# Optimization experiments

Hardware: AMD Instinct MI355X
Metric: run time of the kernel (lower is better)

Reference implementation:

```python
import jax, jax.numpy as jnp
import numpy as np

NUM_USER = 20000
NUM_ITEM = 40000
N_NODES = NUM_USER + NUM_ITEM
DIM = 64
V_DIM = 2048
T_DIM = 768
N_EDGES = 1_000_000
K_USER = 40
K_ITEM = 10
N_LAYERS = 2


def setup_inputs() -> dict:
    key = jax.random.key(0)
    ks = iter(jax.random.split(key, 32))

    def xavier(shape):
        s = (2.0 / (shape[0] + shape[-1])) ** 0.5
        return jax.random.normal(next(ks), shape, jnp.float32) * s

    # bipartite user-item interactions, doubled (undirected), as in DRAGON.__init__
    u = jax.random.randint(next(ks), (N_EDGES,), 0, NUM_USER)
    it = jax.random.randint(next(ks), (N_EDGES,), NUM_USER, N_NODES)
    edge_index = jnp.stack([jnp.concatenate([u, it]), jnp.concatenate([it, u])])

    v_feat = jax.random.normal(next(ks), (NUM_ITEM, V_DIM), jnp.float32)
    t_feat = jax.random.normal(next(ks), (NUM_ITEM, T_DIM), jnp.float32)

    # KNN item-item adjacency (top-10 per row) with symmetric-normalized values,
    # mirroring get_knn_adj_mat/compute_normalized_laplacian
    rows = jnp.repeat(jnp.arange(NUM_ITEM), K_ITEM)
    cols = jax.random.randint(next(ks), (NUM_ITEM * K_ITEM,), 0, NUM_ITEM)
    mm_indices = jnp.stack([rows, cols])
    row_sum = jax.ops.segment_sum(jnp.ones(NUM_ITEM * K_ITEM, jnp.float32), rows,
                                  num_segments=NUM_ITEM) + 1e-7
    rinv = row_sum ** -0.5
    mm_values = rinv[rows] * rinv[cols]

    user_graph = jax.random.randint(next(ks), (NUM_USER, K_USER), 0, NUM_USER)
    user_weight_matrix = jax.nn.softmax(
        jax.random.normal(next(ks), (NUM_USER, K_USER), jnp.float32), axis=1)
    weight_u = jax.nn.softmax(
        jax.random.normal(next(ks), (NUM_USER, 2, 1), jnp.float32), axis=1)

    return {
        'edge_index': edge_index,
        'v_feat': v_feat, 't_feat': t_feat,
        'v_pref': xavier((NUM_USER, DIM)), 't_pref': xavier((NUM_USER, DIM)),
        'v_mlp1_w': xavier((V_DIM, 4 * DIM)), 'v_mlp1_b': jnp.zeros(4 * DIM, jnp.float32),
        'v_mlp2_w': xavier((4 * DIM, DIM)), 'v_mlp2_b': jnp.zeros(DIM, jnp.float32),
        't_mlp1_w': xavier((T_DIM, 4 * DIM)), 't_mlp1_b': jnp.zeros(4 * DIM, jnp.float32),
        't_mlp2_w': xavier((4 * DIM, DIM)), 't_mlp2_b': jnp.zeros(DIM, jnp.float32),
        'v_conv_w': xavier((DIM, DIM)), 'v_conv_b': jnp.zeros(DIM, jnp.float32),
        't_conv_w': xavier((DIM, DIM)), 't_conv_b': jnp.zeros(DIM, jnp.float32),
        'weight_u': weight_u,
        'user_graph': user_graph,
        'user_weight_matrix': user_weight_matrix,
        'mm_indices': mm_indices,
        'mm_values': mm_values,
    }


def _l2n(x):
    n = jnp.linalg.norm(x, axis=-1, keepdims=True)
    return x / jnp.maximum(n, 1e-12)


def reference(edge_index, v_feat, t_feat, v_pref, t_pref,
              v_mlp1_w, v_mlp1_b, v_mlp2_w, v_mlp2_b,
              t_mlp1_w, t_mlp1_b, t_mlp2_w, t_mlp2_b,
              v_conv_w, v_conv_b, t_conv_w, t_conv_b,
              weight_u, user_graph, user_weight_matrix,
              mm_indices, mm_values):
    seg = jax.ops.segment_sum
    # GCNConv normalization with self-loops (shared by both branches)
    sl = jnp.arange(N_NODES)
    src = jnp.concatenate([edge_index[0], sl])
    dst = jnp.concatenate([edge_index[1], sl])
    deg = seg(jnp.ones_like(dst, dtype=jnp.float32), dst, num_segments=N_NODES)
    dinv = deg ** -0.5
    norm = (dinv[src] * dinv[dst])[:, None]

    def conv(x, w, b):  # out[dst] += norm * (x @ w)[src], then bias
        return seg(norm * (x @ w)[src], dst, num_segments=N_NODES) + b

    def branch(feat, pref, w1, b1, w2, b2, cw, cb):
        temp = jax.nn.leaky_relu(feat @ w1 + b1) @ w2 + b2  # [I, D]
        x = _l2n(jnp.concatenate([pref, temp], axis=0))      # [N, D]
        h = conv(x, cw, cb)
        h1 = conv(h, cw, cb)
        return x + h + h1

    v_rep = branch(v_feat, v_pref, v_mlp1_w, v_mlp1_b, v_mlp2_w, v_mlp2_b, v_conv_w, v_conv_b)
    t_rep = branch(t_feat, t_pref, t_mlp1_w, t_mlp1_b, t_mlp2_w, t_mlp2_b, t_conv_w, t_conv_b)

    representation = jnp.concatenate([v_rep, t_rep], axis=1)  # [N, 2D]
    wu = weight_u[:, :, 0]  # [U, 2]
    user_rep = jnp.concatenate([wu[:, 0:1] * v_rep[:NUM_USER],
                                wu[:, 1:2] * t_rep[:NUM_USER]], axis=1)  # [U, 2D]
    item_rep = representation[NUM_USER:]  # [I, 2D]

    # User_Graph_sample: weighted sum over sampled user neighborhoods
    h_u = jnp.einsum('uk,ukd->ud', user_weight_matrix, user_rep[user_graph])
    user_rep = user_rep + h_u

    # n_layers of sparse Laplacian propagation over KNN item-item graph
    row, col = mm_indices[0], mm_indices[1]
    h_i = item_rep
    for _ in range(N_LAYERS):
        h_i = seg(mm_values[:, None] * h_i[col], row, num_segments=NUM_ITEM)
    item_rep = item_rep + h_i

    return jnp.concatenate([user_rep, item_rep], axis=0)  # [N, 2D]
```

## Files before the change

kernel.cpp:

```cpp
#include <hip/hip_runtime.h>

#define NUSER 20000
#define NITEM 40000
#define NNODE 60000
#define DIM   64
#define NE    1000000
#define KUSER 40
#define KITEM 10

typedef __attribute__((ext_vector_type(8))) short short8v;
typedef __attribute__((ext_vector_type(4))) float floatx4;

__device__ inline short bf16rne(float f) {
    unsigned u = __builtin_bit_cast(unsigned, f);
    unsigned r = (u + 0x7fffu + ((u >> 16) & 1u)) >> 16;
    return (short)r;
}
__device__ inline unsigned cvt_pk_bf16(float lo, float hi) {
    unsigned r;
    asm("v_cvt_pk_bf16_f32 %0, %1, %2" : "=v"(r) : "v"(lo), "v"(hi));
    return r;
}
__device__ inline float bflo(unsigned v) { return __builtin_bit_cast(float, v << 16); }
__device__ inline float bfhi(unsigned v) { return __builtin_bit_cast(float, v & 0xffff0000u); }

__global__ __launch_bounds__(256) void k_count(const int* __restrict__ dst, int* __restrict__ cnt, int n) {
    int i = blockIdx.x * 256 + threadIdx.x;
    if (i < n) atomicAdd(&cnt[dst[i]], 1);
}

__global__ __launch_bounds__(256) void k_dinv(const int* __restrict__ cnt, float* __restrict__ dinv) {
    int i = blockIdx.x * 256 + threadIdx.x;
    if (i < NNODE) dinv[i] = 1.0f / sqrtf((float)(cnt[i] + 1));
}

__global__ __launch_bounds__(256) void k_scanA(const int* __restrict__ v, int* __restrict__ excl,
                                               int* __restrict__ bsum, int n) {
    __shared__ int s[256];
    int t = threadIdx.x, i = blockIdx.x * 256 + t;
    int orig = (i < n) ? v[i] : 0;
    s[t] = orig; __syncthreads();
    #pragma unroll
    for (int off = 1; off < 256; off <<= 1) {
        int u = (t >= off) ? s[t - off] : 0;
        __syncthreads();
        s[t] += u;
        __syncthreads();
    }
    if (i < n) excl[i] = s[t] - orig;
    if (t == 255) bsum[blockIdx.x] = s[255];
}

__global__ __launch_bounds__(256) void k_scanB(int* __restrict__ bsum, int nb) {
    __shared__ int s[256];
    int t = threadIdx.x;
    int orig = (t < nb) ? bsum[t] : 0;
    s[t] = orig; __syncthreads();
    #pragma unroll
    for (int off = 1; off < 256; off <<= 1) {
        int u = (t >= off) ? s[t - off] : 0;
        __syncthreads();
        s[t] += u;
        __syncthreads();
    }
    if (t < nb) bsum[t] = s[t] - orig;
}

__global__ __launch_bounds__(256) void k_scanC(int* __restrict__ excl, const int* __restrict__ bsum,
                                               int* __restrict__ cursor, int n) {
    int i = blockIdx.x * 256 + threadIdx.x;
    if (i < n) {
        int v = excl[i] + bsum[blockIdx.x];
        excl[i] = v;
        cursor[i] = v;
    }
    if (i == 0) excl[n] = 2 * NE;
}

__global__ __launch_bounds__(256) void k_fill(const int* __restrict__ src, const int* __restrict__ dst,
                                              const float* __restrict__ dinv, int* __restrict__ cursor,
                                              unsigned* __restrict__ csr_pkd, int n) {
    int i = blockIdx.x * 256 + threadIdx.x;
    if (i >= n) return;
    int s = src[i], d = dst[i];
    unsigned pk = ((unsigned)(unsigned short)bf16rne(dinv[s]) << 16) | (unsigned)s;
    int pos = atomicAdd(&cursor[d], 1);
    csr_pkd[pos] = pk;
}

__global__ __launch_bounds__(256) void k_transpose_bf16(const float* __restrict__ B, short* __restrict__ Btb,
                                                        int K, int N) {
    __shared__ float s[16][17];
    int t = threadIdx.x, tx = t & 15, ty = t >> 4;
    int k0 = blockIdx.x * 16, n0 = blockIdx.y * 16;
    s[ty][tx] = B[(size_t)(k0 + ty) * N + n0 + tx];
    __syncthreads();
    int k = k0 + tx, n = n0 + ty;
    Btb[(size_t)(k >> 5) * (N * 32) + n * 32 + (k & 31)] = bf16rne(s[tx][ty]);
}

#define AP   40
#define MIDP 264
__global__ __launch_bounds__(256) void mlp_fused(const float* __restrict__ A, const short* __restrict__ B1t,
                                                 const float* __restrict__ b1, const short* __restrict__ B2t,
                                                 const float* __restrict__ b2, float* __restrict__ X, int K) {
    __shared__ short smem[2 * 64 * AP + 2 * 256 * AP];
    short* As = smem;
    short* Bs = smem + 2 * 64 * AP;
    const int tid = threadIdx.x;
    const int lane = tid & 63, wid = tid >> 6;
    const int rowBase = blockIdx.x * 64;

    const int sar = tid >> 2, sac = (tid & 3) * 8;
    const float* aptr = A + (size_t)(rowBase + sar) * K + sac;

    const int fk = (lane >> 4) * 8;
    const int faoff = (lane & 15) * AP + fk;
    const int fboff = (wid * 64 + (lane & 15)) * AP + fk;

    floatx4 acc[4][4];
    #pragma unroll
    for (int m = 0; m < 4; m++)
        #pragma unroll
        for (int n = 0; n < 4; n++) acc[m][n] = (floatx4)0.f;

    float4 ra0, ra1;
    short8v rb[4];
    const int nk = K >> 5;

    auto ldg = [&](int ks) {
        const float* ap = aptr + ks * 32;
        ra0 = *(const float4*)(ap);
        ra1 = *(const float4*)(ap + 4);
        const short* bsrc = B1t + (size_t)ks * 8192 + tid * 8;
        #pragma unroll
        for (int it = 0; it < 4; it++) rb[it] = *(const short8v*)(bsrc + it * 2048);
    };
    auto stv = [&](int buf) {
        uint4 av;
        av.x = cvt_pk_bf16(ra0.x, ra0.y); av.y = cvt_pk_bf16(ra0.z, ra0.w);
        av.z = cvt_pk_bf16(ra1.x, ra1.y); av.w = cvt_pk_bf16(ra1.z, ra1.w);
        *(uint4*)&As[buf * (64 * AP) + sar * AP + sac] = av;
        #pragma unroll
        for (int it = 0; it < 4; it++)
            *(short8v*)&Bs[buf * (256 * AP) + (sar + it * 64) * AP + sac] = rb[it];
    };

    ldg(0); stv(0);
    __syncthreads();
    int cur = 0;
    for (int ks = 0; ks < nk; ++ks) {
        if (ks + 1 < nk) ldg(ks + 1);
        short8v a[4], b[4];
        #pragma unroll
        for (int m = 0; m < 4; m++) a[m] = *(const short8v*)&As[cur * (64 * AP) + faoff + m * 16 * AP];
        #pragma unroll
        for (int n = 0; n < 4; n++) b[n] = *(const short8v*)&Bs[cur * (256 * AP) + fboff + n * 16 * AP];
        #pragma unroll
        for (int m = 0; m < 4; m++)
            #pragma unroll
            for (int n = 0; n < 4; n++)
                acc[m][n] = __builtin_amdgcn_mfma_f32_16x16x32_bf16(a[m], b[n], acc[m][n], 0, 0, 0);
        if (ks + 1 < nk) stv(cur ^ 1);
        __syncthreads();
        cur ^= 1;
    }

    short* mid = Bs;
    float bcol[4];
    #pragma unroll
    for (int n = 0; n < 4; n++) bcol[n] = b1[wid * 64 + n * 16 + (lane & 15)];
    #pragma unroll
    for (int m = 0; m < 4; m++)
        #pragma unroll
        for (int n = 0; n < 4; n++)
            #pragma unroll
            for (int q = 0; q < 4; q++) {
                int row = m * 16 + (lane >> 4) * 4 + q;
                int col = wid * 64 + n * 16 + (lane & 15);
                float v = acc[m][n][q] + bcol[n];
                v = v > 0.f ? v : 0.01f * v;
                mid[row * MIDP + col] = bf16rne(v);
            }
    __syncthreads();

    floatx4 acc2[4];
    #pragma unroll
    for (int n2 = 0; n2 < 4; n2++) acc2[n2] = (floatx4)0.f;
    const int arow = wid * 16 + (lane & 15);
    #pragma unroll
    for (int ks2 = 0; ks2 < 8; ++ks2) {
        short8v af = *(const short8v*)&mid[arow * MIDP + ks2 * 32 + fk];
        const short* bp = B2t + ks2 * 2048 + fk;
        short8v bf4[4];
        #pragma unroll
        for (int n2 = 0; n2 < 4; n2++) bf4[n2] = *(const short8v*)(bp + (n2 * 16 + (lane & 15)) * 32);
        #pragma unroll
        for (int n2 = 0; n2 < 4; n2++)
            acc2[n2] = __builtin_amdgcn_mfma_f32_16x16x32_bf16(af, bf4[n2], acc2[n2], 0, 0, 0);
    }

    float b2c[4];
    #pragma unroll
    for (int n2 = 0; n2 < 4; n2++) b2c[n2] = b2[n2 * 16 + (lane & 15)];
    #pragma unroll
    for (int q = 0; q < 4; ++q) {
        float v[4]; float ss = 0.f;
        #pragma unroll
        for (int n2 = 0; n2 < 4; n2++) { v[n2] = acc2[n2][q] + b2c[n2]; ss += v[n2] * v[n2]; }
        ss += __shfl_xor(ss, 1, 64);
        ss += __shfl_xor(ss, 2, 64);
        ss += __shfl_xor(ss, 4, 64);
        ss += __shfl_xor(ss, 8, 64);
        float sc = 1.f / fmaxf(sqrtf(ss), 1e-12f);
        int grow = rowBase + wid * 16 + (lane >> 4) * 4 + q;
        #pragma unroll
        for (int n2 = 0; n2 < 4; n2++)
            X[(size_t)grow * 64 + n2 * 16 + (lane & 15)] = v[n2] * sc;
    }
}

__global__ __launch_bounds__(256) void k_l2n_pref(const float* __restrict__ prefv, const float* __restrict__ preft,
                                                  float* __restrict__ xv, float* __restrict__ xt) {
    int row = blockIdx.x * 4 + (threadIdx.x >> 6);
    int lane = threadIdx.x & 63;
    if (row >= NUSER) return;
    const float* p = blockIdx.y ? preft : prefv;
    float* x = blockIdx.y ? xt : xv;
    float v = p[(size_t)row * 64 + lane];
    float ss = v * v;
    #pragma unroll
    for (int off = 32; off >= 1; off >>= 1) ss += __shfl_xor(ss, off, 64);
    x[(size_t)row * 64 + lane] = v / fmaxf(sqrtf(ss), 1e-12f);
}

__global__ __launch_bounds__(256) void conv_dual(const float* __restrict__ A0, const float* __restrict__ A1,
                                                 int lda, const float* __restrict__ Bv, const float* __restrict__ Bt2,
                                                 unsigned short* __restrict__ Ch) {
    __shared__ float As2[16][65];
    __shared__ float Bs2[16][65];
    const float* A = blockIdx.y ? A1 : A0;
    const float* B = blockIdx.y ? Bt2 : Bv;
    const int colOff = (int)blockIdx.y * 64;
    const int tid = threadIdx.x;
    const int tx = tid & 15, ty = tid >> 4;
    const int rowBase = blockIdx.x * 64;
    float acc[4][4] = {};
    for (int k0 = 0; k0 < 64; k0 += 16) {
        {
            int r = tid >> 2, c = (tid & 3) * 4;
            int gr = rowBase + r;
            float4 v = make_float4(0.f, 0.f, 0.f, 0.f);
            if (gr < NNODE) v = *(const float4*)(A + (size_t)gr * lda + k0 + c);
            As2[c + 0][r] = v.x; As2[c + 1][r] = v.y; As2[c + 2][r] = v.z; As2[c + 3][r] = v.w;
        }
        {
            int r = tid >> 4, c = (tid & 15) * 4;
            float4 v = *(const float4*)(B + (size_t)(k0 + r) * 64 + c);
            Bs2[r][c + 0] = v.x; Bs2[r][c + 1] = v.y; Bs2[r][c + 2] = v.z; Bs2[r][c + 3] = v.w;
        }
        __syncthreads();
        #pragma unroll
        for (int k = 0; k < 16; k++) {
            float a[4], b[4];
            #pragma unroll
            for (int i = 0; i < 4; i++) a[i] = As2[k][ty * 4 + i];
            #pragma unroll
            for (int j = 0; j < 4; j++) b[j] = Bs2[k][tx * 4 + j];
            #pragma unroll
            for (int i = 0; i < 4; i++)
                #pragma unroll
                for (int j = 0; j < 4; j++) acc[i][j] += a[i] * b[j];
        }
        __syncthreads();
    }
    const int gr0 = rowBase + ty * 4, gc = tx * 4;
    #pragma unroll
    for (int i = 0; i < 4; i++) {
        if (gr0 + i >= NNODE) break;
        uint2 hh;
        hh.x = cvt_pk_bf16(acc[i][0], acc[i][1]);
        hh.y = cvt_pk_bf16(acc[i][2], acc[i][3]);
        *(uint2*)(Ch + (size_t)(gr0 + i) * 128 + colOff + gc) = hh;
    }
}

__device__ inline float2 gather_row(const int* rowptr, const unsigned* csr_pkd, const unsigned* gw2,
                                    int row, int lane, float dr) {
    int p0 = rowptr[row], p1 = rowptr[row + 1];
    unsigned sv = gw2[(size_t)row * 64 + lane];
    float ax0 = dr * bflo(sv), ay0 = dr * bfhi(sv);
    float ax1 = 0.f, ay1 = 0.f;
    for (int p = p0; p < p1; p += 64) {
        int c = p1 - p; if (c > 64) c = 64;
        unsigned pk = (lane < c) ? csr_pkd[p + lane] : 0u;
        int j = 0;
        for (; j + 4 <= c; j += 4) {
            unsigned e0 = __shfl(pk, j, 64),     e1 = __shfl(pk, j + 1, 64);
            unsigned e2 = __shfl(pk, j + 2, 64), e3 = __shfl(pk, j + 3, 64);
            unsigned v0 = gw2[(size_t)(e0 & 0xffffu) * 64 + lane];
            unsigned v1 = gw2[(size_t)(e1 & 0xffffu) * 64 + lane];
            unsigned v2 = gw2[(size_t)(e2 & 0xffffu) * 64 + lane];
            unsigned v3 = gw2[(size_t)(e3 & 0xffffu) * 64 + lane];
            float w0 = bfhi(e0), w1 = bfhi(e1), w2 = bfhi(e2), w3 = bfhi(e3);
            ax0 += w0 * bflo(v0); ay0 += w0 * bfhi(v0);
            ax1 += w1 * bflo(v1); ay1 += w1 * bfhi(v1);
            ax0 += w2 * bflo(v2); ay0 += w2 * bfhi(v2);
            ax1 += w3 * bflo(v3); ay1 += w3 * bfhi(v3);
        }
        for (; j < c; ++j) {
            unsigned e = __shfl(pk, j, 64);
            unsigned v = gw2[(size_t)(e & 0xffffu) * 64 + lane];
            float w = bfhi(e);
            ax0 += w * bflo(v); ay0 += w * bfhi(v);
        }
    }
    float2 r; r.x = ax0 + ax1; r.y = ay0 + ay1;
    return r;
}

__global__ __launch_bounds__(256) void k_gather2(const int* __restrict__ rowptr, const unsigned* __restrict__ csr_pkd,
                                                 const float* __restrict__ dinv, const unsigned* __restrict__ gw2,
                                                 const float* __restrict__ cbv, const float* __restrict__ cbt,
                                                 float* __restrict__ h2) {
    int row = blockIdx.x * 4 + (threadIdx.x >> 6);
    int lane = threadIdx.x & 63;
    if (row >= NNODE) return;
    float dr = dinv[row];
    float2 g = gather_row(rowptr, csr_pkd, gw2, row, lane, dr);
    int c0 = 2 * lane;
    float b0 = (c0 < 64) ? cbv[c0] : cbt[c0 - 64];
    float b1 = (c0 + 1 < 64) ? cbv[c0 + 1] : cbt[c0 + 1 - 64];
    float2 r;
    r.x = b0 + dr * g.x;
    r.y = b1 + dr * g.y;
    *(float2*)(h2 + (size_t)row * 128 + c0) = r;
}

__global__ __launch_bounds__(256) void k_gather2_rep(const int* __restrict__ rowptr, const unsigned* __restrict__ csr_pkd,
                                                     const float* __restrict__ dinv, const unsigned* __restrict__ gw2,
                                                     const float* __restrict__ cbv, const float* __restrict__ cbt,
                                                     const float* __restrict__ xv, const float* __restrict__ xt,
                                                     const float* __restrict__ h2, const float* __restrict__ weight_u,
                                                     float* __restrict__ rep0, unsigned* __restrict__ rep_bf) {
    int row = blockIdx.x * 4 + (threadIdx.x >> 6);
    int lane = threadIdx.x & 63;
    if (row >= NNODE) return;
    float dr = dinv[row];
    float2 g = gather_row(rowptr, csr_pkd, gw2, row, lane, dr);
    int c0 = 2 * lane;
    float b0 = (c0 < 64) ? cbv[c0] : cbt[c0 - 64];
    float b1 = (c0 + 1 < 64) ? cbv[c0 + 1] : cbt[c0 + 1 - 64];
    float h12x = b0 + dr * g.x;
    float h12y = b1 + dr * g.y;
    const float* x = (lane < 32) ? xv : xt;
    float2 xp = *(const float2*)(x + (size_t)row * 64 + (c0 & 63));
    float2 hp = *(const float2*)(h2 + (size_t)row * 128 + c0);
    float w = (row < NUSER) ? weight_u[row * 2 + (lane >> 5)] : 1.0f;
    float2 rp;
    rp.x = w * (xp.x + hp.x + h12x);
    rp.y = w * (xp.y + hp.y + h12y);
    *(float2*)(rep0 + (size_t)row * 128 + c0) = rp;
    rep_bf[(size_t)row * 64 + lane] = cvt_pk_bf16(rp.x, rp.y);
}

#define UBLK (NUSER * 64 / 256)
__global__ __launch_bounds__(256) void k_user_item1(const float* __restrict__ rep0, const unsigned* __restrict__ rep_bf,
                                                    const int* __restrict__ ug, const float* __restrict__ uwm,
                                                    const int* __restrict__ mm_col, const float* __restrict__ mm_values,
                                                    float* __restrict__ out, unsigned* __restrict__ tmp_bf) {
    int bid = blockIdx.x;
    if (bid < UBLK) {
        int id = bid * 256 + threadIdx.x;
        int u = id >> 6, lane = id & 63;
        float2 acc = *(const float2*)(rep0 + (size_t)u * 128 + 2 * lane);
        #pragma unroll 4
        for (int k = 0; k < KUSER; k++) {
            int nb = ug[u * KUSER + k];
            float w = uwm[u * KUSER + k];
            unsigned v = rep_bf[(size_t)nb * 64 + lane];
            acc.x += w * bflo(v);
            acc.y += w * bfhi(v);
        }
        *(float2*)(out + (size_t)u * 128 + 2 * lane) = acc;
    } else {
        int id = (bid - UBLK) * 256 + threadIdx.x;
        int r = id >> 6, lane = id & 63;
        float ax = 0.f, ay = 0.f;
        #pragma unroll
        for (int j = 0; j < KITEM; j++) {
            int c = mm_col[r * KITEM + j];
            float w = mm_values[r * KITEM + j];
            unsigned v = rep_bf[(size_t)(NUSER + c) * 64 + lane];
            ax += w * bflo(v);
            ay += w * bfhi(v);
        }
        tmp_bf[(size_t)r * 64 + lane] = cvt_pk_bf16(ax, ay);
    }
}

__global__ __launch_bounds__(256) void k_item2(const float* __restrict__ rep0, const unsigned* __restrict__ tmp_bf,
                                               const int* __restrict__ mm_col, const float* __restrict__ mm_values,
                                               float* __restrict__ out) {
    int id = blockIdx.x * 256 + threadIdx.x;
    int r = id >> 6, lane = id & 63;
    if (r >= NITEM) return;
    float ax = 0.f, ay = 0.f;
    #pragma unroll
    for (int j = 0; j < KITEM; j++) {
        int c = mm_col[r * KITEM + j];
        float w = mm_values[r * KITEM + j];
        unsigned v = tmp_bf[(size_t)c * 64 + lane];
        ax += w * bflo(v);
        ay += w * bfhi(v);
    }
    float2 base = *(const float2*)(rep0 + (size_t)(NUSER + r) * 128 + 2 * lane);
    float2 o;
    o.x = base.x + ax;
    o.y = base.y + ay;
    *(float2*)(out + (size_t)(NUSER + r) * 128 + 2 * lane) = o;
}

extern "C" void kernel_launch(void* const* d_in, const int* in_sizes, int n_in,
                              void* d_out, int out_size, void* d_ws, size_t ws_size,
                              hipStream_t stream) {
    const int*   edge_index = (const int*)d_in[0];
    const float* v_feat   = (const float*)d_in[1];
    const float* t_feat   = (const float*)d_in[2];
    const float* v_pref   = (const float*)d_in[3];
    const float* t_pref   = (const float*)d_in[4];
    const float* v_mlp1_w = (const float*)d_in[5];
    const float* v_mlp1_b = (const float*)d_in[6];
    const float* v_mlp2_w = (const float*)d_in[7];
    const float* v_mlp2_b = (const float*)d_in[8];
    const float* t_mlp1_w = (const float*)d_in[9];
    const float* t_mlp1_b = (const float*)d_in[10];
    const float* t_mlp2_w = (const float*)d_in[11];
    const float* t_mlp2_b = (const float*)d_in[12];
    const float* v_conv_w = (const float*)d_in[13];
    const float* v_conv_b = (const float*)d_in[14];
    const float* t_conv_w = (const float*)d_in[15];
    const float* t_conv_b = (const float*)d_in[16];
    const float* weight_u = (const float*)d_in[17];
    const int*   user_graph = (const int*)d_in[18];
    const float* uwm      = (const float*)d_in[19];
    const int*   mm_indices = (const int*)d_in[20];
    const float* mm_values  = (const float*)d_in[21];
    float* out = (float*)d_out;

    char* wsb = (char*)d_ws;
    size_t off = 0;
    auto alloc = [&](size_t bytes) -> void* {
        void* p = wsb + off;
        off = (off + bytes + 255) & ~(size_t)255;
        return p;
    };
    int*      cnt     = (int*)     alloc(NNODE * 4);
    float*    dinv    = (float*)   alloc(NNODE * 4);
    int*      rowptr  = (int*)     alloc((NNODE + 1) * 4);
    int*      bsum    = (int*)     alloc(256 * 4);
    int*      cursor  = (int*)     alloc(NNODE * 4);
    unsigned* csr_pkd = (unsigned*)alloc((size_t)2 * NE * 4);
    short*    Btw     = (short*)   alloc((size_t)2048 * 256 * 2);
    short*    W2b     = (short*)   alloc((size_t)256 * 64 * 2);
    float*    xv      = (float*)   alloc((size_t)NNODE * DIM * 4);
    float*    xt      = (float*)   alloc((size_t)NNODE * DIM * 4);
    unsigned short* gw2 = (unsigned short*)alloc((size_t)NNODE * 128 * 2);
    float*    h2      = (float*)   alloc((size_t)NNODE * 128 * 4);
    float*    rep0    = (float*)   alloc((size_t)NNODE * 128 * 4);
    unsigned* rep_bf  = (unsigned*)alloc((size_t)NNODE * 64 * 4);
    unsigned* tmp_bf  = (unsigned*)alloc((size_t)NITEM * 64 * 4);
    (void)ws_size; (void)n_in; (void)in_sizes; (void)out_size;

    const int* e_src = edge_index;
    const int* e_dst = edge_index + 2 * NE;
    const int* mm_col = mm_indices + NITEM * KITEM;

    const int NB = (NNODE + 255) / 256;

    hipMemsetAsync(cnt, 0, NNODE * 4, stream);
    k_count<<<(2 * NE + 255) / 256, 256, 0, stream>>>(e_dst, cnt, 2 * NE);
    k_dinv<<<(NNODE + 255) / 256, 256, 0, stream>>>(cnt, dinv);
    k_scanA<<<NB, 256, 0, stream>>>(cnt, rowptr, bsum, NNODE);
    k_scanB<<<1, 256, 0, stream>>>(bsum, NB);
    k_scanC<<<NB, 256, 0, stream>>>(rowptr, bsum, cursor, NNODE);
    k_fill<<<(2 * NE + 255) / 256, 256, 0, stream>>>(e_src, e_dst, dinv, cursor, csr_pkd, 2 * NE);

    {
        dim3 t1(2048 / 16, 16);
        k_transpose_bf16<<<t1, 256, 0, stream>>>(v_mlp1_w, Btw, 2048, 256);
        dim3 t2(256 / 16, 4);
        k_transpose_bf16<<<t2, 256, 0, stream>>>(v_mlp2_w, W2b, 256, 64);
        mlp_fused<<<NITEM / 64, 256, 0, stream>>>(v_feat, Btw, v_mlp1_b, W2b, v_mlp2_b,
                                                  xv + (size_t)NUSER * DIM, 2048);
        dim3 t3(768 / 16, 16);
        k_transpose_bf16<<<t3, 256, 0, stream>>>(t_mlp1_w, Btw, 768, 256);
        k_transpose_bf16<<<t2, 256, 0, stream>>>(t_mlp2_w, W2b, 256, 64);
        mlp_fused<<<NITEM / 64, 256, 0, stream>>>(t_feat, Btw, t_mlp1_b, W2b, t_mlp2_b,
                                                  xt + (size_t)NUSER * DIM, 768);
    }
    {
        dim3 g(NUSER / 4, 2);
        k_l2n_pref<<<g, 256, 0, stream>>>(v_pref, t_pref, xv, xt);
    }

    {
        dim3 g((NNODE + 63) / 64, 2);
        conv_dual<<<g, 256, 0, stream>>>(xv, xt, DIM, v_conv_w, t_conv_w, gw2);
        k_gather2<<<(NNODE + 3) / 4, 256, 0, stream>>>(rowptr, csr_pkd, dinv, (const unsigned*)gw2,
                                                       v_conv_b, t_conv_b, h2);
        conv_dual<<<g, 256, 0, stream>>>(h2, h2 + 64, 128, v_conv_w, t_conv_w, gw2);
        k_gather2_rep<<<(NNODE + 3) / 4, 256, 0, stream>>>(rowptr, csr_pkd, dinv, (const unsigned*)gw2,
                                                           v_conv_b, t_conv_b, xv, xt, h2, weight_u,
                                                           rep0, rep_bf);
    }

    k_user_item1<<<UBLK + NITEM * 64 / 256, 256, 0, stream>>>(rep0, rep_bf, user_graph, uwm,
                                                              mm_col, mm_values, out, tmp_bf);
    k_item2<<<NITEM * 64 / 256, 256, 0, stream>>>(rep0, tmp_bf, mm_col, mm_values, out);
}
```

Measured before the change: 600.2 us.

## Reassociate graph convolutions: propagate first, then apply combined weight GEMM

Uses linearity of the conv layers to propagate the normalized features through the graph twice (bf16 gathers), then applies one fused MFMA GEMM against a concatenated [W; W·W] matrix with precomputed bias terms (b·W scaled by a per-row degree sum, plus 2b). This replaces two fp32 SIMT conv GEMMs and the fp32 intermediate h2 buffer with a single tensor-core GEMM. The MLP and l2-norm kernels now also emit bf16 copies so the gathers can read packed data directly. The cost is an extra tiny single-block prep kernel and a different rounding order, since bf16 propagation now happens before the weight multiply.

New measurement: 627.4 us. 1.05x slower.

```diff
diff --git a/kernel.cpp b/kernel.cpp
--- a/kernel.cpp
+++ b/kernel.cpp
@@ -99,11 +99,52 @@
     Btb[(size_t)(k >> 5) * (N * 32) + n * 32 + (k & 31)] = bf16rne(s[tx][ty]);
 }
 
+__global__ __launch_bounds__(256) void k_prep(const float* __restrict__ Wv, const float* __restrict__ Wt,
+                                              const float* __restrict__ bv, const float* __restrict__ bt,
+                                              short* __restrict__ Bcat, float* __restrict__ bw, float* __restrict__ bb) {
+    __shared__ float Wld[2][64][65];
+    __shared__ float W2ld[2][64][65];
+    int t = threadIdx.x;
+    for (int id = t; id < 8192; id += 256) {
+        int z = id >> 12, k = (id >> 6) & 63, n = id & 63;
+        Wld[z][k][n] = (z ? Wt : Wv)[k * 64 + n];
+    }
+    __syncthreads();
+    for (int id = t; id < 8192; id += 256) {
+        int z = id >> 12, k = (id >> 6) & 63, n = id & 63;
+        float a = 0.f;
+        #pragma unroll 8
+        for (int m = 0; m < 64; m++) a += Wld[z][k][m] * Wld[z][m][n];
+        W2ld[z][k][n] = a;
+    }
+    __syncthreads();
+    for (int id = t; id < 32768; id += 256) {
+        int k = id >> 7, n = id & 127;
+        int kb = k >> 6, kk = k & 63;
+        float v = 0.f;
+        if (kb == 0)      { if (n < 64)  v = Wld[0][kk][n]; }
+        else if (kb == 1) { if (n >= 64) v = Wld[1][kk][n - 64]; }
+        else if (kb == 2) { if (n < 64)  v = W2ld[0][kk][n]; }
+        else              { if (n >= 64) v = W2ld[1][kk][n - 64]; }
+        Bcat[(k >> 5) * 4096 + n * 32 + (k & 31)] = bf16rne(v);
+    }
+    if (t < 128) {
+        int z = t >> 6, n = t & 63;
+        const float* b = z ? bt : bv;
+        float a = 0.f;
+        #pragma unroll 8
+        for (int k = 0; k < 64; k++) a += b[k] * Wld[z][k][n];
+        bw[t] = a;
+        bb[t] = 2.f * b[n];
+    }
+}
+
 #define AP   40
 #define MIDP 264
 __global__ __launch_bounds__(256) void mlp_fused(const float* __restrict__ A, const short* __restrict__ B1t,
                                                  const float* __restrict__ b1, const short* __restrict__ B2t,
-                                                 const float* __restrict__ b2, float* __restrict__ X, int K) {
+                                                 const float* __restrict__ b2, float* __restrict__ X,
+                                                 unsigned* __restrict__ xbf, int boff, int K) {
     __shared__ short smem[2 * 64 * AP + 2 * 256 * AP];
     short* As = smem;
     short* Bs = smem + 2 * 64 * AP;
@@ -215,13 +256,19 @@
         float sc = 1.f / fmaxf(sqrtf(ss), 1e-12f);
         int grow = rowBase + wid * 16 + (lane >> 4) * 4 + q;
         #pragma unroll
-        for (int n2 = 0; n2 < 4; n2++)
-            X[(size_t)grow * 64 + n2 * 16 + (lane & 15)] = v[n2] * sc;
+        for (int n2 = 0; n2 < 4; n2++) {
+            float xn = v[n2] * sc;
+            X[(size_t)grow * 64 + n2 * 16 + (lane & 15)] = xn;
+            float pn = __shfl_xor(xn, 1, 64);
+            if (!(lane & 1))
+                xbf[(size_t)grow * 64 + boff + n2 * 8 + ((lane & 15) >> 1)] = cvt_pk_bf16(xn, pn);
+        }
     }
 }
 
 __global__ __launch_bounds__(256) void k_l2n_pref(const float* __restrict__ prefv, const float* __restrict__ preft,
-                                                  float* __restrict__ xv, float* __restrict__ xt) {
+                                                  float* __restrict__ xv, float* __restrict__ xt,
+                                                  unsigned* __restrict__ xbf) {
     int row = blockIdx.x * 4 + (threadIdx.x >> 6);
     int lane = threadIdx.x & 63;
     if (row >= NUSER) return;
@@ -231,77 +278,38 @@
     float ss = v * v;
     #pragma unroll
     for (int off = 32; off >= 1; off >>= 1) ss += __shfl_xor(ss, off, 64);
-    x[(size_t)row * 64 + lane] = v / fmaxf(sqrtf(ss), 1e-12f);
-}
-
-__global__ __launch_bounds__(256) void conv_dual(const float* __restrict__ A0, const float* __restrict__ A1,
-                                                 int lda, const float* __restrict__ Bv, const float* __restrict__ Bt2,
-                                                 unsigned short* __restrict__ Ch) {
-    __shared__ float As2[16][65];
-    __shared__ float Bs2[16][65];
-    const float* A = blockIdx.y ? A1 : A0;
-    const float* B = blockIdx.y ? Bt2 : Bv;
-    const int colOff = (int)blockIdx.y * 64;
-    const int tid = threadIdx.x;
-    const int tx = tid & 15, ty = tid >> 4;
-    const int rowBase = blockIdx.x * 64;
-    float acc[4][4] = {};
-    for (int k0 = 0; k0 < 64; k0 += 16) {
-        {
-            int r = tid >> 2, c = (tid & 3) * 4;
-            int gr = rowBase + r;
-            float4 v = make_float4(0.f, 0.f, 0.f, 0.f);
-            if (gr < NNODE) v = *(const float4*)(A + (size_t)gr * lda + k0 + c);
-            As2[c + 0][r] = v.x; As2[c + 1][r] = v.y; As2[c + 2][r] = v.z; As2[c + 3][r] = v.w;
-        }
-        {
-            int r = tid >> 4, c = (tid & 15) * 4;
-            float4 v = *(const float4*)(B + (size_t)(k0 + r) * 64 + c);
-            Bs2[r][c + 0] = v.x; Bs2[r][c + 1] = v.y; Bs2[r][c + 2] = v.z; Bs2[r][c + 3] = v.w;
-        }
-        __syncthreads();
-        #pragma unroll
-        for (int k = 0; k < 16; k++) {
-            float a[4], b[4];
-            #pragma unroll
-            for (int i = 0; i < 4; i++) a[i] = As2[k][ty * 4 + i];
-            #pragma unroll
-            for (int j = 0; j < 4; j++) b[j] = Bs2[k][tx * 4 + j];
-            #pragma unroll
-            for (int i = 0; i < 4; i++)
-                #pragma unroll
-                for (int j = 0; j < 4; j++) acc[i][j] += a[i] * b[j];
-        }
-        __syncthreads();
-    }
-    const int gr0 = rowBase + ty * 4, gc = tx * 4;
-    #pragma unroll
-    for (int i = 0; i < 4; i++) {
-        if (gr0 + i >= NNODE) break;
-        uint2 hh;
-        hh.x = cvt_pk_bf16(acc[i][0], acc[i][1]);
-        hh.y = cvt_pk_bf16(acc[i][2], acc[i][3]);
-        *(uint2*)(Ch + (size_t)(gr0 + i) * 128 + colOff + gc) = hh;
-    }
-}
-
-__device__ inline float2 gather_row(const int* rowptr, const unsigned* csr_pkd, const unsigned* gw2,
-                                    int row, int lane, float dr) {
+    float xn = v / fmaxf(sqrtf(ss), 1e-12f);
+    x[(size_t)row * 64 + lane] = xn;
+    float pn = __shfl_xor(xn, 1, 64);
+    if (!(lane & 1))
+        xbf[(size_t)row * 64 + (blockIdx.y ? 32 : 0) + (lane >> 1)] = cvt_pk_bf16(xn, pn);
+}
+
+template<bool WITH_S>
+__global__ __launch_bounds__(256) void k_gather_p(const int* __restrict__ rowptr, const unsigned* __restrict__ csr_pkd,
+                                                  const float* __restrict__ dinv, const unsigned* __restrict__ in_bf,
+                                                  unsigned* __restrict__ out_bf, float* __restrict__ s_out) {
+    int row = blockIdx.x * 4 + (threadIdx.x >> 6);
+    int lane = threadIdx.x & 63;
+    if (row >= NNODE) return;
     int p0 = rowptr[row], p1 = rowptr[row + 1];
-    unsigned sv = gw2[(size_t)row * 64 + lane];
+    float dr = dinv[row];
+    unsigned sv = in_bf[(size_t)row * 64 + lane];
     float ax0 = dr * bflo(sv), ay0 = dr * bfhi(sv);
     float ax1 = 0.f, ay1 = 0.f;
+    float wsum = 0.f;
     for (int p = p0; p < p1; p += 64) {
         int c = p1 - p; if (c > 64) c = 64;
         unsigned pk = (lane < c) ? csr_pkd[p + lane] : 0u;
+        if (WITH_S) wsum += bfhi(pk);
         int j = 0;
         for (; j + 4 <= c; j += 4) {
             unsigned e0 = __shfl(pk, j, 64),     e1 = __shfl(pk, j + 1, 64);
             unsigned e2 = __shfl(pk, j + 2, 64), e3 = __shfl(pk, j + 3, 64);
-            unsigned v0 = gw2[(size_t)(e0 & 0xffffu) * 64 + lane];
-            unsigned v1 = gw2[(size_t)(e1 & 0xffffu) * 64 + lane];
-            unsigned v2 = gw2[(size_t)(e2 & 0xffffu) * 64 + lane];
-            unsigned v3 = gw2[(size_t)(e3 & 0xffffu) * 64 + lane];
+            unsigned v0 = in_bf[(size_t)(e0 & 0xffffu) * 64 + lane];
+            unsigned v1 = in_bf[(size_t)(e1 & 0xffffu) * 64 + lane];
+            unsigned v2 = in_bf[(size_t)(e2 & 0xffffu) * 64 + lane];
+            unsigned v3 = in_bf[(size_t)(e3 & 0xffffu) * 64 + lane];
             float w0 = bfhi(e0), w1 = bfhi(e1), w2 = bfhi(e2), w3 = bfhi(e3);
             ax0 += w0 * bflo(v0); ay0 += w0 * bfhi(v0);
             ax1 += w1 * bflo(v1); ay1 += w1 * bfhi(v1);
@@ -310,58 +318,73 @@
         }
         for (; j < c; ++j) {
             unsigned e = __shfl(pk, j, 64);
-            unsigned v = gw2[(size_t)(e & 0xffffu) * 64 + lane];
+            unsigned v = in_bf[(size_t)(e & 0xffffu) * 64 + lane];
             float w = bfhi(e);
             ax0 += w * bflo(v); ay0 += w * bfhi(v);
         }
     }
-    float2 r; r.x = ax0 + ax1; r.y = ay0 + ay1;
-    return r;
-}
-
-__global__ __launch_bounds__(256) void k_gather2(const int* __restrict__ rowptr, const unsigned* __restrict__ csr_pkd,
-                                                 const float* __restrict__ dinv, const unsigned* __restrict__ gw2,
-                                                 const float* __restrict__ cbv, const float* __restrict__ cbt,
-                                                 float* __restrict__ h2) {
-    int row = blockIdx.x * 4 + (threadIdx.x >> 6);
-    int lane = threadIdx.x & 63;
-    if (row >= NNODE) return;
-    float dr = dinv[row];
-    float2 g = gather_row(rowptr, csr_pkd, gw2, row, lane, dr);
-    int c0 = 2 * lane;
-    float b0 = (c0 < 64) ? cbv[c0] : cbt[c0 - 64];
-    float b1 = (c0 + 1 < 64) ? cbv[c0 + 1] : cbt[c0 + 1 - 64];
-    float2 r;
-    r.x = b0 + dr * g.x;
-    r.y = b1 + dr * g.y;
-    *(float2*)(h2 + (size_t)row * 128 + c0) = r;
-}
-
-__global__ __launch_bounds__(256) void k_gather2_rep(const int* __restrict__ rowptr, const unsigned* __restrict__ csr_pkd,
-                                                     const float* __restrict__ dinv, const unsigned* __restrict__ gw2,
-                                                     const float* __restrict__ cbv, const float* __restrict__ cbt,
-                                                     const float* __restrict__ xv, const float* __restrict__ xt,
-                                                     const float* __restrict__ h2, const float* __restrict__ weight_u,
-                                                     float* __restrict__ rep0, unsigned* __restrict__ rep_bf) {
-    int row = blockIdx.x * 4 + (threadIdx.x >> 6);
-    int lane = threadIdx.x & 63;
-    if (row >= NNODE) return;
-    float dr = dinv[row];
-    float2 g = gather_row(rowptr, csr_pkd, gw2, row, lane, dr);
-    int c0 = 2 * lane;
-    float b0 = (c0 < 64) ? cbv[c0] : cbt[c0 - 64];
-    float b1 = (c0 + 1 < 64) ? cbv[c0 + 1] : cbt[c0 + 1 - 64];
-    float h12x = b0 + dr * g.x;
-    float h12y = b1 + dr * g.y;
-    const float* x = (lane < 32) ? xv : xt;
-    float2 xp = *(const float2*)(x + (size_t)row * 64 + (c0 & 63));
-    float2 hp = *(const float2*)(h2 + (size_t)row * 128 + c0);
-    float w = (row < NUSER) ? weight_u[row * 2 + (lane >> 5)] : 1.0f;
-    float2 rp;
-    rp.x = w * (xp.x + hp.x + h12x);
-    rp.y = w * (xp.y + hp.y + h12y);
-    *(float2*)(rep0 + (size_t)row * 128 + c0) = rp;
-    rep_bf[(size_t)row * 64 + lane] = cvt_pk_bf16(rp.x, rp.y);
+    out_bf[(size_t)row * 64 + lane] = cvt_pk_bf16(dr * (ax0 + ax1), dr * (ay0 + ay1));
+    if (WITH_S) {
+        #pragma unroll
+        for (int o = 32; o >= 1; o >>= 1) wsum += __shfl_xor(wsum, o, 64);
+        if (lane == 0) s_out[row] = dr * (dr + wsum);
+    }
+}
+
+__global__ __launch_bounds__(256) void k_rep_gemm(const unsigned* __restrict__ g1, const unsigned* __restrict__ g2,
+                                                  const short* __restrict__ Bcat,
+                                                  const float* __restrict__ xv, const float* __restrict__ xt,
+                                                  const float* __restrict__ s, const float* __restrict__ bw,
+                                                  const float* __restrict__ bb, const float* __restrict__ weight_u,
+                                                  float* __restrict__ rep0, unsigned* __restrict__ rep_bf) {
+    __shared__ short Alds[64 * 264];
+    const int tid = threadIdx.x, lane = tid & 63, wid = tid >> 6;
+    const int rowBase = blockIdx.x * 64;
+    #pragma unroll
+    for (int i = 0; i < 8; i++) {
+        int cid = tid + i * 256;
+        int r = cid >> 5, c = cid & 31;
+        int grow = rowBase + r; if (grow >= NNODE) grow = NNODE - 1;
+        const unsigned* src = (c < 16) ? (g1 + (size_t)grow * 64 + c * 4)
+                                       : (g2 + (size_t)grow * 64 + (c - 16) * 4);
+        uint4 v = *(const uint4*)src;
+        *(uint4*)&Alds[r * 264 + c * 8] = v;
+    }
+    __syncthreads();
+    const int fk = (lane >> 4) * 8;
+    const int arow = wid * 16 + (lane & 15);
+    floatx4 acc[8];
+    #pragma unroll
+    for (int n = 0; n < 8; n++) acc[n] = (floatx4)0.f;
+    #pragma unroll
+    for (int ks = 0; ks < 8; ks++) {
+        short8v af = *(const short8v*)&Alds[arow * 264 + ks * 32 + fk];
+        #pragma unroll
+        for (int n = 0; n < 8; n++) {
+            short8v bf = *(const short8v*)(Bcat + ks * 4096 + (n * 16 + (lane & 15)) * 32 + fk);
+            acc[n] = __builtin_amdgcn_mfma_f32_16x16x32_bf16(af, bf, acc[n], 0, 0, 0);
+        }
+    }
+    #pragma unroll
+    for (int n = 0; n < 8; n++) {
+        int col = n * 16 + (lane & 15);
+        float bwc = bw[col], bbc = bb[col];
+        #pragma unroll
+        for (int q = 0; q < 4; q++) {
+            int row = rowBase + wid * 16 + (lane >> 4) * 4 + q;
+            int rc = row < NNODE ? row : NNODE - 1;
+            float xval = (col < 64) ? xv[(size_t)rc * 64 + col] : xt[(size_t)rc * 64 + col - 64];
+            float v = acc[n][q] + xval + s[rc] * bwc + bbc;
+            float w = (rc < NUSER) ? weight_u[rc * 2 + (col >> 6)] : 1.0f;
+            v *= w;
+            float pn = __shfl_xor(v, 1, 64);
+            if (row < NNODE) {
+                rep0[(size_t)row * 128 + col] = v;
+                if (!(lane & 1))
+                    rep_bf[(size_t)row * 64 + n * 8 + ((lane & 15) >> 1)] = cvt_pk_bf16(v, pn);
+            }
+        }
+    }
 }
 
 #define UBLK (NUSER * 64 / 256)
@@ -463,10 +486,15 @@
     unsigned* csr_pkd = (unsigned*)alloc((size_t)2 * NE * 4);
     short*    Btw     = (short*)   alloc((size_t)2048 * 256 * 2);
     short*    W2b     = (short*)   alloc((size_t)256 * 64 * 2);
+    short*    Bcat    = (short*)   alloc((size_t)256 * 128 * 2);
+    float*    bw      = (float*)   alloc(128 * 4);
+    float*    bb      = (float*)   alloc(128 * 4);
+    float*    svec    = (float*)   alloc(NNODE * 4);
     float*    xv      = (float*)   alloc((size_t)NNODE * DIM * 4);
     float*    xt      = (float*)   alloc((size_t)NNODE * DIM * 4);
-    unsigned short* gw2 = (unsigned short*)alloc((size_t)NNODE * 128 * 2);
-    float*    h2      = (float*)   alloc((size_t)NNODE * 128 * 4);
+    unsigned* x_bf    = (unsigned*)alloc((size_t)NNODE * 64 * 4);
+    unsigned* g1      = (unsigned*)alloc((size_t)NNODE * 64 * 4);
+    unsigned* g2      = (unsigned*)alloc((size_t)NNODE * 64 * 4);
     float*    rep0    = (float*)   alloc((size_t)NNODE * 128 * 4);
     unsigned* rep_bf  = (unsigned*)alloc((size_t)NNODE * 64 * 4);
     unsigned* tmp_bf  = (unsigned*)alloc((size_t)NITEM * 64 * 4);
@@ -486,34 +514,30 @@
     k_scanC<<<NB, 256, 0, stream>>>(rowptr, bsum, cursor, NNODE);
     k_fill<<<(2 * NE + 255) / 256, 256, 0, stream>>>(e_src, e_dst, dinv, cursor, csr_pkd, 2 * NE);
 
+    k_prep<<<1, 256, 0, stream>>>(v_conv_w, t_conv_w, v_conv_b, t_conv_b, Bcat, bw, bb);
+
     {
         dim3 t1(2048 / 16, 16);
         k_transpose_bf16<<<t1, 256, 0, stream>>>(v_mlp1_w, Btw, 2048, 256);
         dim3 t2(256 / 16, 4);
         k_transpose_bf16<<<t2, 256, 0, stream>>>(v_mlp2_w, W2b, 256, 64);
         mlp_fused<<<NITEM / 64, 256, 0, stream>>>(v_feat, Btw, v_mlp1_b, W2b, v_mlp2_b,
-                                                  xv + (size_t)NUSER * DIM, 2048);
+                                                  xv + (size_t)NUSER * DIM, x_bf + (size_t)NUSER * 64, 0, 2048);
         dim3 t3(768 / 16, 16);
         k_transpose_bf16<<<t3, 256, 0, stream>>>(t_mlp1_w, Btw, 768, 256);
         k_transpose_bf16<<<t2, 256, 0, stream>>>(t_mlp2_w, W2b, 256, 64);
         mlp_fused<<<NITEM / 64, 256, 0, stream>>>(t_feat, Btw, t_mlp1_b, W2b, t_mlp2_b,
-                                                  xt + (size_t)NUSER * DIM, 768);
+                                                  xt + (size_t)NUSER * DIM, x_bf + (size_t)NUSER * 64, 32, 768);
     }
     {
         dim3 g(NUSER / 4, 2);
-        k_l2n_pref<<<g, 256, 0, stream>>>(v_pref, t_pref, xv, xt);
-    }
-
-    {
-        dim3 g((NNODE + 63) / 64, 2);
-        conv_dual<<<g, 256, 0, stream>>>(xv, xt, DIM, v_conv_w, t_conv_w, gw2);
-        k_gather2<<<(NNODE + 3) / 4, 256, 0, stream>>>(rowptr, csr_pkd, dinv, (const unsigned*)gw2,
-                                                       v_conv_b, t_conv_b, h2);
-        conv_dual<<<g, 256, 0, stream>>>(h2, h2 + 64, 128, v_conv_w, t_conv_w, gw2);
-        k_gather2_rep<<<(NNODE + 3) / 4, 256, 0, stream>>>(rowptr, csr_pkd, dinv, (const unsigned*)gw2,
-                                                           v_conv_b, t_conv_b, xv, xt, h2, weight_u,
-                                                           rep0, rep_bf);
-    }
+        k_l2n_pref<<<g, 256, 0, stream>>>(v_pref, t_pref, xv, xt, x_bf);
+    }
+
+    k_gather_p<true><<<(NNODE + 3) / 4, 256, 0, stream>>>(rowptr, csr_pkd, dinv, x_bf, g1, svec);
+    k_gather_p<false><<<(NNODE + 3) / 4, 256, 0, stream>>>(rowptr, csr_pkd, dinv, g1, g2, nullptr);
+    k_rep_gemm<<<(NNODE + 63) / 64, 256, 0, stream>>>(g1, g2, Bcat, xv, xt, svec, bw, bb, weight_u,
+                                                      rep0, rep_bf);
 
     k_user_item1<<<UBLK + NITEM * 64 / 256, 256, 0, stream>>>(rep0, rep_bf, user_graph, uwm,
                                                               mm_col, mm_values, out, tmp_bf);
```
